# Kernel optimization log

Measured on AMD Instinct MI355X. Metric: run time of the kernel, lower is better.

Reference implementation:

```python
import jax, jax.numpy as jnp
import numpy as np

N_NODES = 100000
N_EDGES = 1600000
N_GRAPHS = 1000
H = 4

def _ln(x, g, b, eps=1e-5):
    m = x.mean(-1, keepdims=True)
    v = ((x - m) ** 2).mean(-1, keepdims=True)
    return (x - m) / jnp.sqrt(v + eps) * g + b

def _gat(x, src, dst, W, att_src, att_dst, bias, C):
    # PyG GATConv (self-loops already appended to src/dst): per-edge scores,
    # segment softmax over incoming edges of each dst node, scatter-add aggregation.
    N = x.shape[0]
    h = (x @ W.T).reshape(N, H, C)                      # [N,H,C]
    a_s = (h * att_src[None]).sum(-1)                   # [N,H]
    a_d = (h * att_dst[None]).sum(-1)                   # [N,H]
    e = jax.nn.leaky_relu(a_s[src] + a_d[dst], 0.2)     # [E,H]
    m = jax.ops.segment_max(e, dst, num_segments=N)
    w = jnp.exp(e - m[dst])
    denom = jax.ops.segment_sum(w, dst, num_segments=N)
    alpha = w / denom[dst]
    out = jax.ops.segment_sum(alpha[:, :, None] * h[src], dst, num_segments=N)
    return out.reshape(N, H * C) + bias

def _mha_len1(y, in_w, in_b, out_w, out_b, d):
    # seq_len==1 (x.unsqueeze(0)): softmax over a single key is identically 1,
    # so MHA(y,y,y) == out_proj(v_proj(y)). Exactly the original math.
    v = y @ in_w[2 * d:3 * d].T + in_b[2 * d:3 * d]
    return v @ out_w.T + out_b

def _forward(x, edge_index, batch, fc_feat_w, fc_feat_b,
             gat1_w, gat1_as, gat1_ad, gat1_b,
             gat2_w, gat2_as, gat2_ad, gat2_b,
             enc_in_w, enc_in_b, enc_out_w, enc_out_b,
             enc_f1_w, enc_f1_b, enc_f2_w, enc_f2_b,
             enc_ln1_g, enc_ln1_b, enc_ln2_g, enc_ln2_b,
             dec_sa_in_w, dec_sa_in_b, dec_sa_out_w, dec_sa_out_b,
             dec_ca_in_w, dec_ca_in_b, dec_ca_out_w, dec_ca_out_b,
             dec_f1_w, dec_f1_b, dec_f2_w, dec_f2_b,
             dec_ln1_g, dec_ln1_b, dec_ln2_g, dec_ln2_b, dec_ln3_g, dec_ln3_b,
             fc_w, fc_b):
    N = x.shape[0]
    d = 16 * H  # 64
    loop = jnp.arange(N, dtype=edge_index.dtype)
    src = jnp.concatenate([edge_index[0], loop])  # add_self_loops=True (PyG default)
    dst = jnp.concatenate([edge_index[1], loop])
    h = x @ fc_feat_w.T + fc_feat_b                     # feature_fc: [N,8]
    h = jax.nn.leaky_relu(_gat(h, src, dst, gat1_w, gat1_as, gat1_ad, gat1_b, 32), 0.01)
    h = jax.nn.leaky_relu(_gat(h, src, dst, gat2_w, gat2_as, gat2_ad, gat2_b, 16), 0.01)
    y = h  # [N,64]; transformer sees (L=1, B=N, E=64)
    for i in range(2):  # encoder layers
        a = _mha_len1(y, enc_in_w[i], enc_in_b[i], enc_out_w[i], enc_out_b[i], d)
        y = _ln(y + a, enc_ln1_g[i], enc_ln1_b[i])
        f = jax.nn.relu(y @ enc_f1_w[i].T + enc_f1_b[i]) @ enc_f2_w[i].T + enc_f2_b[i]
        y = _ln(y + f, enc_ln2_g[i], enc_ln2_b[i])
    for i in range(2):  # decoder layers (memory == tgt)
        a = _mha_len1(y, dec_sa_in_w[i], dec_sa_in_b[i], dec_sa_out_w[i], dec_sa_out_b[i], d)
        y = _ln(y + a, dec_ln1_g[i], dec_ln1_b[i])
        a = _mha_len1(y, dec_ca_in_w[i], dec_ca_in_b[i], dec_ca_out_w[i], dec_ca_out_b[i], d)
        y = _ln(y + a, dec_ln2_g[i], dec_ln2_b[i])
        f = jax.nn.relu(y @ dec_f1_w[i].T + dec_f1_b[i]) @ dec_f2_w[i].T + dec_f2_b[i]
        y = _ln(y + f, dec_ln3_g[i], dec_ln3_b[i])
    sums = jax.ops.segment_sum(y, batch, num_segments=N_GRAPHS)
    cnts = jax.ops.segment_sum(jnp.ones((N,), y.dtype), batch, num_segments=N_GRAPHS)
    pooled = sums / jnp.maximum(cnts, 1.0)[:, None]     # global_mean_pool
    return pooled @ fc_w.T + fc_b

def setup_inputs() -> dict:
    key = jax.random.key(0)
    ks = iter(jax.random.split(key, 64))
    p = lambda *s: jax.random.normal(next(ks), s, dtype=jnp.float32) * 0.1
    d = 64
    inp = {
        'x': jax.random.normal(next(ks), (N_NODES, 4), dtype=jnp.float32),
        'edge_index': jax.random.randint(next(ks), (2, N_EDGES), 0, N_NODES, dtype=jnp.int32),
        'batch': jnp.sort(jax.random.randint(next(ks), (N_NODES,), 0, N_GRAPHS, dtype=jnp.int32)),
        'fc_feat_w': p(8, 4), 'fc_feat_b': p(8),
        'gat1_w': p(128, 8), 'gat1_as': p(H, 32), 'gat1_ad': p(H, 32), 'gat1_b': p(128),
        'gat2_w': p(64, 128), 'gat2_as': p(H, 16), 'gat2_ad': p(H, 16), 'gat2_b': p(64),
        'enc_in_w': p(2, 3 * d, d), 'enc_in_b': p(2, 3 * d), 'enc_out_w': p(2, d, d), 'enc_out_b': p(2, d),
        'enc_f1_w': p(2, 256, d), 'enc_f1_b': p(2, 256), 'enc_f2_w': p(2, d, 256), 'enc_f2_b': p(2, d),
        'enc_ln1_g': jnp.ones((2, d)), 'enc_ln1_b': jnp.zeros((2, d)),
        'enc_ln2_g': jnp.ones((2, d)), 'enc_ln2_b': jnp.zeros((2, d)),
        'dec_sa_in_w': p(2, 3 * d, d), 'dec_sa_in_b': p(2, 3 * d), 'dec_sa_out_w': p(2, d, d), 'dec_sa_out_b': p(2, d),
        'dec_ca_in_w': p(2, 3 * d, d), 'dec_ca_in_b': p(2, 3 * d), 'dec_ca_out_w': p(2, d, d), 'dec_ca_out_b': p(2, d),
        'dec_f1_w': p(2, 256, d), 'dec_f1_b': p(2, 256), 'dec_f2_w': p(2, d, 256), 'dec_f2_b': p(2, d),
        'dec_ln1_g': jnp.ones((2, d)), 'dec_ln1_b': jnp.zeros((2, d)),
        'dec_ln2_g': jnp.ones((2, d)), 'dec_ln2_b': jnp.zeros((2, d)),
        'dec_ln3_g': jnp.ones((2, d)), 'dec_ln3_b': jnp.zeros((2, d)),
        'fc_w': p(33, d), 'fc_b': p(33),
    }
    return inp

def reference(x, edge_index, batch, fc_feat_w, fc_feat_b,
              gat1_w, gat1_as, gat1_ad, gat1_b,
              gat2_w, gat2_as, gat2_ad, gat2_b,
              enc_in_w, enc_in_b, enc_out_w, enc_out_b,
              enc_f1_w, enc_f1_b, enc_f2_w, enc_f2_b,
              enc_ln1_g, enc_ln1_b, enc_ln2_g, enc_ln2_b,
              dec_sa_in_w, dec_sa_in_b, dec_sa_out_w, dec_sa_out_b,
              dec_ca_in_w, dec_ca_in_b, dec_ca_out_w, dec_ca_out_b,
              dec_f1_w, dec_f1_b, dec_f2_w, dec_f2_b,
              dec_ln1_g, dec_ln1_b, dec_ln2_g, dec_ln2_b, dec_ln3_g, dec_ln3_b,
              fc_w, fc_b):
    return _forward(x, edge_index, batch, fc_feat_w, fc_feat_b,
                    gat1_w, gat1_as, gat1_ad, gat1_b,
                    gat2_w, gat2_as, gat2_ad, gat2_b,
                    enc_in_w, enc_in_b, enc_out_w, enc_out_b,
                    enc_f1_w, enc_f1_b, enc_f2_w, enc_f2_b,
                    enc_ln1_g, enc_ln1_b, enc_ln2_g, enc_ln2_b,
                    dec_sa_in_w, dec_sa_in_b, dec_sa_out_w, dec_sa_out_b,
                    dec_ca_in_w, dec_ca_in_b, dec_ca_out_w, dec_ca_out_b,
                    dec_f1_w, dec_f1_b, dec_f2_w, dec_f2_b,
                    dec_ln1_g, dec_ln1_b, dec_ln2_g, dec_ln2_b, dec_ln3_g, dec_ln3_b,
                    fc_w, fc_b)
```

## Files before the change

### kernel.cpp

```cpp
#include <hip/hip_runtime.h>

#define NN 100000
#define NE 1600000
#define NG 1000
#define ETOT (NE + NN)
#define NODES_PER_GRP 12500

typedef _Float16 f16x8 __attribute__((ext_vector_type(8)));
typedef _Float16 f16x4 __attribute__((ext_vector_type(4)));
typedef _Float16 f16x2 __attribute__((ext_vector_type(2)));
typedef float f32x16 __attribute__((ext_vector_type(16)));
#define XROW 72

__global__ void k_h1(const float* __restrict__ x, const float* __restrict__ ffw,
                     const float* __restrict__ ffb, const float* __restrict__ g1w,
                     const float* __restrict__ asw, const float* __restrict__ adw,
                     _Float16* __restrict__ h1p, float* __restrict__ asp,
                     float* __restrict__ ad_) {
    int tid = blockIdx.x * 256 + threadIdx.x;
    int n = __builtin_amdgcn_readfirstlane(tid >> 6);
    int jp = threadIdx.x & 63;
    float xv[4];
#pragma unroll
    for (int k = 0; k < 4; k++) xv[k] = x[n * 4 + k];
    float h0[8];
#pragma unroll
    for (int o = 0; o < 8; o++) {
        float a = ffb[o];
#pragma unroll
        for (int k = 0; k < 4; k++) a = fmaf(xv[k], ffw[o * 4 + k], a);
        h0[o] = a;
    }
    const float* w0 = g1w + jp * 8;
    const float* w1 = g1w + (jp + 64) * 8;
    float a0 = 0.f, a1 = 0.f;
#pragma unroll
    for (int k = 0; k < 8; k++) { a0 = fmaf(h0[k], w0[k], a0); a1 = fmaf(h0[k], w1[k], a1); }
    f16x2 r; r[0] = (_Float16)a0; r[1] = (_Float16)a1;
    *(f16x2*)(h1p + ((size_t)n * 64 + jp) * 2) = r;
    float p0 = a0 * asw[jp], p1 = a1 * asw[jp + 64];
    float d0 = a0 * adw[jp], d1 = a1 * adw[jp + 64];
#pragma unroll
    for (int m = 1; m <= 16; m <<= 1) {
        p0 += __shfl_xor(p0, m, 64); p1 += __shfl_xor(p1, m, 64);
        d0 += __shfl_xor(d0, m, 64); d1 += __shfl_xor(d1, m, 64);
    }
    if ((jp & 31) == 0) {
        int half = jp >> 5;
        *(float2*)(asp + n * 4 + half * 2) = make_float2(p0, p1);
        ad_[n * 4 + half] = d0;
        ad_[n * 4 + 2 + half] = d1;
    }
}

__global__ void k_att2(const _Float16* __restrict__ h2h, const float* __restrict__ asw,
                       const float* __restrict__ adw, float* __restrict__ as_,
                       float* __restrict__ ad_) {
    int tid = blockIdx.x * 256 + threadIdx.x;
    if (tid >= NN * 4) return;
    int n = tid >> 2, h = tid & 3;
    const _Float16* hp = h2h + (size_t)n * 64 + h * 16;
    const float* ws_ = asw + h * 16;
    const float* wd_ = adw + h * 16;
    float a = 0.f, d = 0.f;
#pragma unroll
    for (int c = 0; c < 16; c++) {
        float hv = (float)hp[c];
        a = fmaf(hv, ws_[c], a); d = fmaf(hv, wd_[c], d);
    }
    as_[tid] = a; ad_[tid] = d;
}

__global__ void k_count(const int* __restrict__ ei, int* __restrict__ deg) {
    int g = blockIdx.x & 7;
    int bi = blockIdx.x >> 3;
    int nb = gridDim.x >> 3;
    int lo = g * NODES_PER_GRP, hi = lo + NODES_PER_GRP;
    for (int e = bi * 256 + threadIdx.x; e < NE; e += nb * 256) {
        int dst = __builtin_nontemporal_load(ei + NE + e);
        if (dst >= lo && dst < hi) atomicAdd(&deg[dst], 1);
    }
}

__global__ void k_scan1(const int* __restrict__ deg, int* __restrict__ offs, int* __restrict__ bsum) {
    __shared__ int s[1024];
    int tid = threadIdx.x;
    int i = blockIdx.x * 1024 + tid;
    int v = (i < NN) ? deg[i] + 1 : 0;
    s[tid] = v;
    __syncthreads();
    for (int d = 1; d < 1024; d <<= 1) {
        int t = 0;
        if (tid >= d) t = s[tid - d];
        __syncthreads();
        if (tid >= d) s[tid] += t;
        __syncthreads();
    }
    if (i < NN) offs[i] = s[tid] - v;
    if (tid == 1023) bsum[blockIdx.x] = s[tid];
}

__global__ void k_scan2(int* __restrict__ bsum) {
    __shared__ int s[128];
    int tid = threadIdx.x;
    int v = (tid < 98) ? bsum[tid] : 0;
    s[tid] = v;
    __syncthreads();
    for (int d = 1; d < 128; d <<= 1) {
        int t = 0;
        if (tid >= d) t = s[tid - d];
        __syncthreads();
        if (tid >= d) s[tid] += t;
        __syncthreads();
    }
    bsum[tid] = s[tid] - v;
}

__global__ void k_scan3(int* __restrict__ offs, const int* __restrict__ bsum, int* __restrict__ cur,
                        int* __restrict__ srcs) {
    int i = blockIdx.x * 1024 + threadIdx.x;
    if (i < NN) {
        int v = offs[i] + bsum[blockIdx.x];
        offs[i] = v;
        cur[i] = v + 1;
        srcs[v] = i;
    }
    if (i == 0) offs[NN] = ETOT;
}

__global__ void k_scatter(const int* __restrict__ ei, int* __restrict__ cur,
                          int* __restrict__ srcs) {
    int g = blockIdx.x & 7;
    int bi = blockIdx.x >> 3;
    int nb = gridDim.x >> 3;
    int lo = g * NODES_PER_GRP, hi = lo + NODES_PER_GRP;
    for (int e = bi * 256 + threadIdx.x; e < NE; e += nb * 256) {
        int dst = __builtin_nontemporal_load(ei + NE + e);
        if (dst >= lo && dst < hi) {
            int src = __builtin_nontemporal_load(ei + e);
            int p = atomicAdd(&cur[dst], 1);
            srcs[p] = src;
        }
    }
}

__global__ void k_ew1(const int* __restrict__ offs, const int* __restrict__ srcs,
                      const float* __restrict__ asp, const float* __restrict__ ad_,
                      uint2* __restrict__ ew) {
    int t = blockIdx.x * 256 + threadIdx.x;
    int d = t >> 4, li = t & 15;
    if (d >= NN) return;
    int off = offs[d], deg = offs[d + 1] - off;
    float4 b = *(const float4*)(ad_ + d * 4);
    for (int j = li; j < deg; j += 16) {
        int s = srcs[off + j];
        float4 a = *(const float4*)(asp + s * 4);
        float e0 = a.x + b.x; e0 = fmaxf(e0, 0.2f * e0);
        float e2 = a.y + b.z; e2 = fmaxf(e2, 0.2f * e2);
        float e1 = a.z + b.y; e1 = fmaxf(e1, 0.2f * e1);
        float e3 = a.w + b.w; e3 = fmaxf(e3, 0.2f * e3);
        union { unsigned u; _Float16 h[2]; } c0, c1;
        c0.h[0] = (_Float16)__expf(e0); c0.h[1] = (_Float16)__expf(e2);
        c1.h[0] = (_Float16)__expf(e1); c1.h[1] = (_Float16)__expf(e3);
        uint2 o; o.x = c0.u; o.y = c1.u;
        ew[off + j] = o;
    }
}

__global__ void k_ew2(const int* __restrict__ offs, const int* __restrict__ srcs,
                      const float* __restrict__ as_, const float* __restrict__ ad_,
                      uint2* __restrict__ ew) {
    int t = blockIdx.x * 256 + threadIdx.x;
    int d = t >> 4, li = t & 15;
    if (d >= NN) return;
    int off = offs[d], deg = offs[d + 1] - off;
    float4 b = *(const float4*)(ad_ + d * 4);
    for (int j = li; j < deg; j += 16) {
        int s = srcs[off + j];
        float4 a = *(const float4*)(as_ + s * 4);
        float e0 = a.x + b.x; e0 = fmaxf(e0, 0.2f * e0);
        float e1 = a.y + b.y; e1 = fmaxf(e1, 0.2f * e1);
        float e2 = a.z + b.z; e2 = fmaxf(e2, 0.2f * e2);
        float e3 = a.w + b.w; e3 = fmaxf(e3, 0.2f * e3);
        union { unsigned u; _Float16 h[2]; } c0, c1;
        c0.h[0] = (_Float16)__expf(e0); c0.h[1] = (_Float16)__expf(e1);
        c1.h[0] = (_Float16)__expf(e2); c1.h[1] = (_Float16)__expf(e3);
        uint2 o; o.x = c0.u; o.y = c1.u;
        ew[off + j] = o;
    }
}

#define G1LD(q)  int s##q = sp[j + q]; uint2 e##q = wp[j + q];
#define G1LDM(q) int jj##q = j + q; int jc##q = jj##q < deg ? jj##q : deg - 1; \
                 int s##q = sp[jc##q]; uint2 e##q = wp[jc##q]; \
                 if (jj##q >= deg) { e##q.x = 0u; e##q.y = 0u; }
#define G1GA(q)  f16x2 p##q = *(const f16x2*)(h1p + (size_t)s##q * 128 + lane * 2);
#define G1AC(q, W0, W1, A0, A1) { \
    union { unsigned u; _Float16 h[2]; } c; c.u = hA ? e##q.y : e##q.x; \
    float w0 = (float)c.h[0], w1 = (float)c.h[1]; \
    W0 += w0; W1 += w1; \
    A0 = fmaf(w0, (float)p##q[0], A0); A1 = fmaf(w1, (float)p##q[1], A1); }

__global__ void k_gat1(const int* __restrict__ offs, const int* __restrict__ srcs,
                       const uint2* __restrict__ ew, const _Float16* __restrict__ h1p,
                       const float* __restrict__ bias, _Float16* __restrict__ g1h) {
    int wid = __builtin_amdgcn_readfirstlane((blockIdx.x * 256 + threadIdx.x) >> 6);
    int lane = threadIdx.x & 63;
    if (wid >= NN) return;
    int off = offs[wid];
    int deg = offs[wid + 1] - off;
    int hA = lane >> 5;
    const int* sp = srcs + off;
    const uint2* wp = ew + off;
    float ws0 = 0.f, ws1 = 0.f, ac0 = 0.f, ac1 = 0.f;
    float ws0b = 0.f, ws1b = 0.f, ac0b = 0.f, ac1b = 0.f;
    int j = 0;
    for (; j + 8 <= deg; j += 8) {
        G1LD(0) G1LD(1) G1LD(2) G1LD(3) G1LD(4) G1LD(5) G1LD(6) G1LD(7)
        G1GA(0) G1GA(1) G1GA(2) G1GA(3) G1GA(4) G1GA(5) G1GA(6) G1GA(7)
        G1AC(0, ws0, ws1, ac0, ac1)     G1AC(1, ws0b, ws1b, ac0b, ac1b)
        G1AC(2, ws0, ws1, ac0, ac1)     G1AC(3, ws0b, ws1b, ac0b, ac1b)
        G1AC(4, ws0, ws1, ac0, ac1)     G1AC(5, ws0b, ws1b, ac0b, ac1b)
        G1AC(6, ws0, ws1, ac0, ac1)     G1AC(7, ws0b, ws1b, ac0b, ac1b)
    }
    if (j < deg) {
        G1LDM(0) G1LDM(1) G1LDM(2) G1LDM(3) G1LDM(4) G1LDM(5) G1LDM(6) G1LDM(7)
        G1GA(0) G1GA(1) G1GA(2) G1GA(3) G1GA(4) G1GA(5) G1GA(6) G1GA(7)
        G1AC(0, ws0, ws1, ac0, ac1)     G1AC(1, ws0b, ws1b, ac0b, ac1b)
        G1AC(2, ws0, ws1, ac0, ac1)     G1AC(3, ws0b, ws1b, ac0b, ac1b)
        G1AC(4, ws0, ws1, ac0, ac1)     G1AC(5, ws0b, ws1b, ac0b, ac1b)
        G1AC(6, ws0, ws1, ac0, ac1)     G1AC(7, ws0b, ws1b, ac0b, ac1b)
    }
    ws0 += ws0b; ws1 += ws1b; ac0 += ac0b; ac1 += ac1b;
    float v0 = ac0 / ws0 + bias[lane];      v0 = fmaxf(v0, 0.01f * v0);
    float v1 = ac1 / ws1 + bias[lane + 64]; v1 = fmaxf(v1, 0.01f * v1);
    g1h[(size_t)wid * 128 + lane] = (_Float16)v0;
    g1h[(size_t)wid * 128 + lane + 64] = (_Float16)v1;
}

#define G2LD(q)  int s##q = sp[j + q]; uint2 e##q = wp[j + q];
#define G2LDM(q) int jj##q = j + q; int jc##q = jj##q < deg ? jj##q : deg - 1; \
                 int s##q = sp[jc##q]; uint2 e##q = wp[jc##q]; \
                 if (jj##q >= deg) { e##q.x = 0u; e##q.y = 0u; }
#define G2GA(q)  float hv##q = (float)h2h[(size_t)s##q * 64 + lane];
#define G2AC(q, W, A) { \
    unsigned sel = (hd & 2) ? e##q.y : e##q.x; \
    union { unsigned u; _Float16 h[2]; } c; c.u = sel >> sh; \
    float w = (float)c.h[0]; W += w; A = fmaf(w, hv##q, A); }

__global__ void k_gat2(const int* __restrict__ offs, const int* __restrict__ srcs,
                       const uint2* __restrict__ ew, const _Float16* __restrict__ h2h,
                       const float* __restrict__ bias, _Float16* __restrict__ g2h) {
    int wid = __builtin_amdgcn_readfirstlane((blockIdx.x * 256 + threadIdx.x) >> 6);
    int lane = threadIdx.x & 63;
    if (wid >= NN) return;
    int off = offs[wid];
    int deg = offs[wid + 1] - off;
    int hd = lane >> 4;
    int sh = (hd & 1) * 16;
    const int* sp = srcs + off;
    const uint2* wp = ew + off;
    float ws = 0.f, ac = 0.f, wsb = 0.f, acb = 0.f;
    int j = 0;
    for (; j + 8 <= deg; j += 8) {
        G2LD(0) G2LD(1) G2LD(2) G2LD(3) G2LD(4) G2LD(5) G2LD(6) G2LD(7)
        G2GA(0) G2GA(1) G2GA(2) G2GA(3) G2GA(4) G2GA(5) G2GA(6) G2GA(7)
        G2AC(0, ws, ac)  G2AC(1, wsb, acb)
        G2AC(2, ws, ac)  G2AC(3, wsb, acb)
        G2AC(4, ws, ac)  G2AC(5, wsb, acb)
        G2AC(6, ws, ac)  G2AC(7, wsb, acb)
    }
    if (j < deg) {
        G2LDM(0) G2LDM(1) G2LDM(2) G2LDM(3) G2LDM(4) G2LDM(5) G2LDM(6) G2LDM(7)
        G2GA(0) G2GA(1) G2GA(2) G2GA(3) G2GA(4) G2GA(5) G2GA(6) G2GA(7)
        G2AC(0, ws, ac)  G2AC(1, wsb, acb)
        G2AC(2, ws, ac)  G2AC(3, wsb, acb)
        G2AC(4, ws, ac)  G2AC(5, wsb, acb)
        G2AC(6, ws, ac)  G2AC(7, wsb, acb)
    }
    ws += wsb; ac += acb;
    float v = ac / ws + bias[lane]; v = fmaxf(v, 0.01f * v);
    g2h[(size_t)wid * 64 + lane] = (_Float16)v;
}

#define GROW 136
#define CROW 72
__global__ __launch_bounds__(256, 2) void k_h2m(const _Float16* __restrict__ g1h,
                                                const _Float16* __restrict__ apw2,
                                                _Float16* __restrict__ h2h) {
    __shared__ _Float16 ls[4 * 32 * GROW];
    const int t = threadIdx.x;
    const int w = t >> 6, l = t & 63;
    const int col = l & 31, hf = l >> 5;
    const int wv = blockIdx.x * 4 + w;
    const int nb = wv * 32;
    if (nb >= NN) return;
    _Float16* g16 = ls + w * (32 * GROW);
    const int r = l >> 1, hb = l & 1;
    {
        int nr = nb + r; if (nr >= NN) nr = NN - 1;
        const _Float16* src = g1h + (size_t)nr * 128 + hb * 64;
        _Float16* dst = g16 + r * GROW + hb * 64;
#pragma unroll
        for (int q = 0; q < 8; q++)
            *(f16x8*)(dst + q * 8) = *(const f16x8*)(src + q * 8);
    }
    f16x8 bf[8];
#pragma unroll
    for (int ks = 0; ks < 8; ks++)
        bf[ks] = *(const f16x8*)(g16 + col * GROW + ks * 16 + hf * 8);
    f32x16 acc0, acc1;
#pragma unroll
    for (int i = 0; i < 16; i++) { acc0[i] = 0.f; acc1[i] = 0.f; }
#pragma unroll
    for (int ks = 0; ks < 8; ks++) {
        f16x8 a0 = *(const f16x8*)(apw2 + ((0 * 8 + ks) * 64 + l) * 8);
        f16x8 a1 = *(const f16x8*)(apw2 + ((1 * 8 + ks) * 64 + l) * 8);
        acc0 = __builtin_amdgcn_mfma_f32_32x32x16_f16(a0, bf[ks], acc0, 0, 0, 0);
        acc1 = __builtin_amdgcn_mfma_f32_32x32x16_f16(a1, bf[ks], acc1, 0, 0, 0);
    }
    _Float16* c16 = g16;
#pragma unroll
    for (int rg = 0; rg < 4; rg++) {
        f16x4 h0, h1;
#pragma unroll
        for (int i = 0; i < 4; i++) { h0[i] = (_Float16)acc0[rg * 4 + i]; h1[i] = (_Float16)acc1[rg * 4 + i]; }
        *(f16x4*)(c16 + col * CROW + rg * 8 + hf * 4) = h0;
        *(f16x4*)(c16 + col * CROW + 32 + rg * 8 + hf * 4) = h1;
    }
    if (nb + r < NN) {
        _Float16* dst = h2h + (size_t)(nb + r) * 64 + hb * 32;
        const _Float16* srow = c16 + r * CROW + hb * 32;
#pragma unroll
        for (int q = 0; q < 4; q++)
            *(f16x8*)(dst + q * 8) = *(const f16x8*)(srow + q * 8);
    }
}

__global__ void k_fuse(const float* __restrict__ enc_in_w, const float* __restrict__ enc_in_b,
                       const float* __restrict__ enc_out_w, const float* __restrict__ enc_out_b,
                       const float* __restrict__ sa_in_w, const float* __restrict__ sa_in_b,
                       const float* __restrict__ sa_out_w, const float* __restrict__ sa_out_b,
                       const float* __restrict__ ca_in_w, const float* __restrict__ ca_in_b,
                       const float* __restrict__ ca_out_w, const float* __restrict__ ca_out_b,
                       _Float16* __restrict__ apk, float* __restrict__ fb) {
    int tid = blockIdx.x * 256 + threadIdx.x;
    int p = tid >> 12, r = tid & 4095, j = r >> 6, k = r & 63;
    int li = p & 1;
    const float *iw, *ib, *ow, *ob;
    if (p < 2)      { iw = enc_in_w + li * 12288; ib = enc_in_b + li * 192; ow = enc_out_w + li * 4096; ob = enc_out_b + li * 64; }
    else if (p < 4) { iw = sa_in_w + li * 12288;  ib = sa_in_b + li * 192;  ow = sa_out_w + li * 4096;  ob = sa_out_b + li * 64; }
    else            { iw = ca_in_w + li * 12288;  ib = ca_in_b + li * 192;  ow = ca_out_w + li * 4096;  ob = ca_out_b + li * 64; }
    float a = 0.f;
    for (int m = 0; m < 64; m++) a = fmaf(ow[j * 64 + m], iw[(128 + m) * 64 + k], a);
    int l = ((k >> 3) & 1) * 32 + (j & 31);
    apk[p * 4096 + (((j >> 5) * 4 + (k >> 4)) * 64 + l) * 8 + (k & 7)] = (_Float16)a;
    if (k == 0) {
        float fa = ob[j];
        for (int m = 0; m < 64; m++) fa = fmaf(ow[j * 64 + m], ib[128 + m], fa);
        fb[p * 64 + j] = fa;
    }
}

#define APK_F1 24576
#define APK_F2 90112
#define APK_TOT 155648
__global__ void k_apack(const float* __restrict__ ef1, const float* __restrict__ df1,
                        const float* __restrict__ ef2, const float* __restrict__ df2,
                        const float* __restrict__ g2w, _Float16* __restrict__ apk,
                        _Float16* __restrict__ apw2) {
    int tid = blockIdx.x * 256 + threadIdx.x;
    if (tid < 65536) {
        int pl = tid >> 14, idx = tid & 16383;
        int mt = idx >> 11, ks = (idx >> 9) & 3, l = (idx >> 3) & 63, d = idx & 7;
        int m = mt * 32 + (l & 31), k = ks * 16 + (l >> 5) * 8 + d;
        const float* f1 = (pl < 2) ? ef1 + pl * 16384 : df1 + (pl - 2) * 16384;
        apk[APK_F1 + pl * 16384 + idx] = (_Float16)f1[m * 64 + k];
    } else if (tid < 131072) {
        int r = tid - 65536;
        int pl = r >> 14, idx = r & 16383;
        int mt = idx >> 13, ks = (idx >> 9) & 15, l = (idx >> 3) & 63, d = idx & 7;
        int m = mt * 32 + (l & 31), k = ks * 16 + (l >> 5) * 8 + d;
        const float* f2 = (pl < 2) ? ef2 + pl * 16384 : df2 + (pl - 2) * 16384;
        apk[APK_F2 + pl * 16384 + idx] = (_Float16)f2[m * 256 + k];
    } else {
        int r = tid - 131072;
        int mtks = r >> 9, l = (r >> 3) & 63, d = r & 7;
        int mt = mtks >> 3, ks = mtks & 7;
        int m = mt * 32 + (l & 31), k = ks * 16 + (l >> 5) * 8 + d;
        apw2[r] = (_Float16)g2w[m * 128 + k];
    }
}

struct XQ {
    const _Float16* apk; const float* fb;
    const float* ef1b; const float* ef2b; const float* df1b; const float* df2b;
    const float* el1g; const float* el1b; const float* el2g; const float* el2b;
    const float* dl1g; const float* dl1b; const float* dl2g; const float* dl2b;
    const float* dl3g; const float* dl3b;
};

__device__ __forceinline__ void xstore(_Float16* xw, const float y[4][16], int col, int hf) {
#pragma unroll
    for (int nt = 0; nt < 2; nt++)
#pragma unroll
        for (int mt = 0; mt < 2; mt++)
#pragma unroll
            for (int rg = 0; rg < 4; rg++) {
                f16x4 h4;
#pragma unroll
                for (int i = 0; i < 4; i++) h4[i] = (_Float16)y[mt * 2 + nt][rg * 4 + i];
                *(f16x4*)(xw + (nt * 32 + col) * XROW + mt * 32 + rg * 8 + hf * 4) = h4;
            }
}

__device__ __forceinline__ void loadbf(const _Float16* xw, f16x8 bf[2][4], int col, int hf) {
#pragma unroll
    for (int nt = 0; nt < 2; nt++)
#pragma unroll
        for (int ks = 0; ks < 4; ks++)
            bf[nt][ks] = *(const f16x8*)(xw + (nt * 32 + col) * XROW + ks * 16 + hf * 8);
}

__device__ __forceinline__ void lnw(float y[4][16], const float* g, const float* b, int hf) {
#pragma unroll
    for (int nt = 0; nt < 2; nt++) {
        float s = 0.f, q = 0.f;
#pragma unroll
        for (int mt = 0; mt < 2; mt++)
#pragma unroll
            for (int r = 0; r < 16; r++) { float v = y[mt * 2 + nt][r]; s += v; q = fmaf(v, v, q); }
        s += __shfl_xor(s, 32, 64);
        q += __shfl_xor(q, 32, 64);
        float m = s * 0.015625f;
        float var = fmaf(q, 0.015625f, -m * m);
        float rs = rsqrtf(var + 1e-5f);
#pragma unroll
        for (int mt = 0; mt < 2; mt++)
#pragma unroll
            for (int rg = 0; rg < 4; rg++) {
                float4 g4 = *(const float4*)(g + mt * 32 + rg * 8 + hf * 4);
                float4 b4 = *(const float4*)(b + mt * 32 + rg * 8 + hf * 4);
                float* yp = &y[mt * 2 + nt][rg * 4];
                yp[0] = fmaf((yp[0] - m) * rs, g4.x, b4.x);
                yp[1] = fmaf((yp[1] - m) * rs, g4.y, b4.y);
                yp[2] = fmaf((yp[2] - m) * rs, g4.z, b4.z);
                yp[3] = fmaf((yp[3] - m) * rs, g4.w, b4.w);
            }
    }
}

__global__ __launch_bounds__(256, 2) void k_xform(const _Float16* __restrict__ yin,
                                                  float* __restrict__ yout, XQ P) {
    __shared__ _Float16 xs[4 * 64 * XROW];
    __shared__ _Float16 wb[8192];
    const int t = threadIdx.x;
    const int w = t >> 6, l = t & 63;
    const int col = l & 31, hf = l >> 5;
    _Float16* xw = xs + w * (64 * XROW);
    const int nb = blockIdx.x * 256 + w * 64;
    const int nn0 = nb + col, nn1 = nb + 32 + col;
    const int nc0 = nn0 < NN ? nn0 : NN - 1;
    const int nc1 = nn1 < NN ? nn1 : NN - 1;

    float y[4][16];
#pragma unroll
    for (int mt = 0; mt < 2; mt++)
#pragma unroll
        for (int nt = 0; nt < 2; nt++) {
            const _Float16* src = yin + (size_t)(nt ? nc1 : nc0) * 64 + mt * 32 + hf * 4;
#pragma unroll
            for (int rg = 0; rg < 4; rg++) {
                f16x4 v = *(const f16x4*)(src + rg * 8);
#pragma unroll
                for (int i = 0; i < 4; i++) y[mt * 2 + nt][rg * 4 + i] = (float)v[i];
            }
        }
    f16x8 bf[2][4];
    xstore(xw, y, col, hf);
    loadbf(xw, bf, col, hf);

#pragma unroll 1
    for (int layer = 0; layer < 4; layer++) {
        const bool enc = layer < 2;
        const int li = enc ? layer : layer - 2;
        const int nat = enc ? 1 : 2;
#pragma unroll 1
        for (int at = 0; at < nat; at++) {
            const int p = enc ? layer : (at == 0 ? 2 + li : 4 + li);
            const _Float16* apA = P.apk + p * 4096;
            __syncthreads();
#pragma unroll
            for (int i = 0; i < 2; i++)
                *(f16x8*)(wb + (t + i * 256) * 8) = *(const f16x8*)(apA + (t + i * 256) * 8);
            __syncthreads();
            const float* fbp = P.fb + p * 64;
            f32x16 acc[4];
#pragma unroll
            for (int mt = 0; mt < 2; mt++) {
                f32x16 a;
#pragma unroll
                for (int rg = 0; rg < 4; rg++) {
                    float4 b4 = *(const float4*)(fbp + mt * 32 + rg * 8 + hf * 4);
                    a[rg * 4 + 0] = b4.x; a[rg * 4 + 1] = b4.y; a[rg * 4 + 2] = b4.z; a[rg * 4 + 3] = b4.w;
                }
                acc[mt * 2 + 0] = a; acc[mt * 2 + 1] = a;
            }
#pragma unroll
            for (int mt = 0; mt < 2; mt++)
#pragma unroll
                for (int ks = 0; ks < 4; ks++) {
                    f16x8 af = *(const f16x8*)(wb + ((mt * 4 + ks) * 64 + l) * 8);
                    acc[mt * 2 + 0] = __builtin_amdgcn_mfma_f32_32x32x16_f16(af, bf[0][ks], acc[mt * 2 + 0], 0, 0, 0);
                    acc[mt * 2 + 1] = __builtin_amdgcn_mfma_f32_32x32x16_f16(af, bf[1][ks], acc[mt * 2 + 1], 0, 0, 0);
                }
#pragma unroll
            for (int ti = 0; ti < 4; ti++)
#pragma unroll
                for (int r = 0; r < 16; r++) y[ti][r] += acc[ti][r];
            const float *g, *b;
            if (enc)          { g = P.el1g + li * 64; b = P.el1b + li * 64; }
            else if (at == 0) { g = P.dl1g + li * 64; b = P.dl1b + li * 64; }
            else              { g = P.dl2g + li * 64; b = P.dl2b + li * 64; }
            lnw(y, g, b, hf);
            xstore(xw, y, col, hf);
            loadbf(xw, bf, col, hf);
        }
        const int pl = enc ? layer : 2 + li;
        const _Float16* apF1 = P.apk + APK_F1 + pl * 16384;
        const _Float16* apF2 = P.apk + APK_F2 + pl * 16384;
        const float* f1bp = (enc ? P.ef1b : P.df1b) + li * 256;
        const float* f2bp = (enc ? P.ef2b : P.df2b) + li * 64;
        f32x16 out[4];
#pragma unroll
        for (int mt = 0; mt < 2; mt++) {
            f32x16 a;
#pragma unroll
            for (int rg = 0; rg < 4; rg++) {
                float4 b4 = *(const float4*)(f2bp + mt * 32 + rg * 8 + hf * 4);
                a[rg * 4 + 0] = b4.x; a[rg * 4 + 1] = b4.y; a[rg * 4 + 2] = b4.z; a[rg * 4 + 3] = b4.w;
            }
            out[mt * 2 + 0] = a; out[mt * 2 + 1] = a;
        }
#pragma unroll 1
        for (int c = 0; c < 4; c++) {
            __syncthreads();
#pragma unroll
            for (int i = 0; i < 2; i++)
                *(f16x8*)(wb + (t + i * 256) * 8) = *(const f16x8*)(apF1 + c * 4096 + (t + i * 256) * 8);
            *(f16x8*)(wb + 4096 + t * 8) = *(const f16x8*)(apF2 + c * 2048 + t * 8);
            *(f16x8*)(wb + 6144 + t * 8) = *(const f16x8*)(apF2 + 8192 + c * 2048 + t * 8);
            __syncthreads();
            f32x16 ha[4];
#pragma unroll
            for (int hmt = 0; hmt < 2; hmt++) {
                f32x16 a;
#pragma unroll
                for (int rg = 0; rg < 4; rg++) {
                    float4 b4 = *(const float4*)(f1bp + c * 64 + hmt * 32 + rg * 8 + hf * 4);
                    a[rg * 4 + 0] = b4.x; a[rg * 4 + 1] = b4.y; a[rg * 4 + 2] = b4.z; a[rg * 4 + 3] = b4.w;
                }
                ha[hmt * 2 + 0] = a; ha[hmt * 2 + 1] = a;
            }
#pragma unroll
            for (int hmt = 0; hmt < 2; hmt++)
#pragma unroll
                for (int ks = 0; ks < 4; ks++) {
                    f16x8 af = *(const f16x8*)(wb + ((hmt * 4 + ks) * 64 + l) * 8);
                    ha[hmt * 2 + 0] = __builtin_amdgcn_mfma_f32_32x32x16_f16(af, bf[0][ks], ha[hmt * 2 + 0], 0, 0, 0);
                    ha[hmt * 2 + 1] = __builtin_amdgcn_mfma_f32_32x32x16_f16(af, bf[1][ks], ha[hmt * 2 + 1], 0, 0, 0);
                }
#pragma unroll
            for (int nt = 0; nt < 2; nt++)
#pragma unroll
                for (int hmt = 0; hmt < 2; hmt++)
#pragma unroll
                    for (int rg = 0; rg < 4; rg++) {
                        f16x4 h4;
#pragma unroll
                        for (int i = 0; i < 4; i++)
                            h4[i] = (_Float16)fmaxf(ha[hmt * 2 + nt][rg * 4 + i], 0.f);
                        *(f16x4*)(xw + (nt * 32 + col) * XROW + hmt * 32 + rg * 8 + hf * 4) = h4;
                    }
#pragma unroll
            for (int ksl = 0; ksl < 4; ksl++) {
                f16x8 hbf0 = *(const f16x8*)(xw + col * XROW + ksl * 16 + hf * 8);
                f16x8 hbf1 = *(const f16x8*)(xw + (32 + col) * XROW + ksl * 16 + hf * 8);
#pragma unroll
                for (int mt = 0; mt < 2; mt++) {
                    f16x8 af = *(const f16x8*)(wb + 4096 + mt * 2048 + (ksl * 64 + l) * 8);
                    out[mt * 2 + 0] = __builtin_amdgcn_mfma_f32_32x32x16_f16(af, hbf0, out[mt * 2 + 0], 0, 0, 0);
                    out[mt * 2 + 1] = __builtin_amdgcn_mfma_f32_32x32x16_f16(af, hbf1, out[mt * 2 + 1], 0, 0, 0);
                }
            }
        }
#pragma unroll
        for (int ti = 0; ti < 4; ti++)
#pragma unroll
            for (int r = 0; r < 16; r++) y[ti][r] += out[ti][r];
        const float* g2 = (enc ? P.el2g : P.dl3g) + li * 64;
        const float* b2 = (enc ? P.el2b : P.dl3b) + li * 64;
        lnw(y, g2, b2, hf);
        if (layer < 3) {
            xstore(xw, y, col, hf);
            loadbf(xw, bf, col, hf);
        }
    }
#pragma unroll
    for (int mt = 0; mt < 2; mt++)
#pragma unroll
        for (int nt = 0; nt < 2; nt++) {
            int n = nt ? nn1 : nn0;
            if (n < NN) {
                float* dst = yout + (size_t)n * 64 + mt * 32 + hf * 4;
#pragma unroll
                for (int rg = 0; rg < 4; rg++) {
                    const float* yp = &y[mt * 2 + nt][rg * 4];
                    *(float4*)(dst + rg * 8) = make_float4(yp[0], yp[1], yp[2], yp[3]);
                }
            }
        }
}

__global__ void k_pool(const float* __restrict__ y, const int* __restrict__ batch,
                       float* __restrict__ pooled) {
    int b = blockIdx.x;
    int t = threadIdx.x;
    int ch = t & 63, r = t >> 6;
    int lo = 0, hi = NN;
    while (lo < hi) { int mid = (lo + hi) >> 1; if (batch[mid] < b) lo = mid + 1; else hi = mid; }
    int st = lo;
    hi = NN;
    while (lo < hi) { int mid = (lo + hi) >> 1; if (batch[mid] < b + 1) lo = mid + 1; else hi = mid; }
    int en = lo;
    float s = 0.f;
    for (int i = st + r; i < en; i += 4) s += y[(size_t)i * 64 + ch];
    __shared__ float red[256];
    red[t] = s;
    __syncthreads();
    if (t < 64) {
        float tot = red[t] + red[t + 64] + red[t + 128] + red[t + 192];
        int cnt = en - st; if (cnt < 1) cnt = 1;
        pooled[b * 64 + t] = tot / (float)cnt;
    }
}

__global__ void k_fc(const float* __restrict__ pooled, const float* __restrict__ fcw,
                     const float* __restrict__ fcb, float* __restrict__ out) {
    int tid = blockIdx.x * 256 + threadIdx.x;
    if (tid >= NG * 33) return;
    int g = tid / 33, o = tid - g * 33;
    const float* p = pooled + g * 64;
    const float* w = fcw + o * 64;
    float a0 = 0.f, a1 = 0.f, a2 = 0.f, a3 = 0.f;
#pragma unroll
    for (int k = 0; k < 16; k++) {
        a0 = fmaf(p[4 * k], w[4 * k], a0);
        a1 = fmaf(p[4 * k + 1], w[4 * k + 1], a1);
        a2 = fmaf(p[4 * k + 2], w[4 * k + 2], a2);
        a3 = fmaf(p[4 * k + 3], w[4 * k + 3], a3);
    }
    out[tid] = fcb[o] + (a0 + a1) + (a2 + a3);
}

extern "C" void kernel_launch(void* const* d_in, const int* in_sizes, int n_in,
                              void* d_out, int out_size, void* d_ws, size_t ws_size,
                              hipStream_t stream) {
    (void)in_sizes; (void)n_in; (void)out_size; (void)ws_size;
    char* ws = (char*)d_ws;
    size_t o = 0;
    auto A = [&](size_t b) { size_t r = o; o += (b + 255) & ~(size_t)255; return r; };
    _Float16* h1p = (_Float16*)(ws + A((size_t)NN * 128 * 2));
    _Float16* h2h = (_Float16*)(ws + A((size_t)NN * 64 * 2));
    _Float16* g1h = (_Float16*)(ws + A((size_t)NN * 128 * 2));
    _Float16* g2h = (_Float16*)(ws + A((size_t)NN * 64 * 2));
    float* f_y   = (float*)(ws + A((size_t)NN * 64 * 4));
    float* f_asp = (float*)(ws + A((size_t)NN * 4 * 4));
    float* f_ad1 = (float*)(ws + A((size_t)NN * 4 * 4));
    float* f_as2 = (float*)(ws + A((size_t)NN * 4 * 4));
    float* f_ad2 = (float*)(ws + A((size_t)NN * 4 * 4));
    int* i_off   = (int*)(ws + A((size_t)(NN + 1) * 4));
    int* i_cur   = (int*)(ws + A((size_t)NN * 4));
    int* i_deg   = (int*)(ws + A((size_t)NN * 4));
    int* i_bsum  = (int*)(ws + A((size_t)1024 * 4));
    int* i_srcs  = (int*)(ws + A((size_t)ETOT * 4));
    uint2* e_w   = (uint2*)(ws + A((size_t)ETOT * 8));
    float* f_fb  = (float*)(ws + A((size_t)6 * 64 * 4));
    _Float16* f_apk = (_Float16*)(ws + A((size_t)APK_TOT * 2));
    _Float16* apw2  = (_Float16*)(ws + A((size_t)8192 * 2));
    float* f_pool= (float*)(ws + A((size_t)NG * 64 * 4));

    const float* x   = (const float*)d_in[0];
    const int* ei    = (const int*)d_in[1];
    const int* batch = (const int*)d_in[2];
    #define F32(i) ((const float*)d_in[i])

    hipMemsetAsync(i_deg, 0, (size_t)NN * 4, stream);
    k_h1<<<NN * 64 / 256, 256, 0, stream>>>(x, F32(3), F32(4), F32(5), F32(6), F32(7),
                                            h1p, f_asp, f_ad1);
    k_count<<<8 * 128, 256, 0, stream>>>(ei, i_deg);
    k_scan1<<<98, 1024, 0, stream>>>(i_deg, i_off, i_bsum);
    k_scan2<<<1, 128, 0, stream>>>(i_bsum);
    k_scan3<<<98, 1024, 0, stream>>>(i_off, i_bsum, i_cur, i_srcs);
    k_scatter<<<8 * 128, 256, 0, stream>>>(ei, i_cur, i_srcs);
    k_ew1<<<NN * 16 / 256, 256, 0, stream>>>(i_off, i_srcs, f_asp, f_ad1, e_w);
    k_gat1<<<NN * 64 / 256, 256, 0, stream>>>(i_off, i_srcs, e_w, h1p, F32(8), g1h);
    k_apack<<<544, 256, 0, stream>>>(F32(17), F32(33), F32(19), F32(35), F32(9), f_apk, apw2);
    k_h2m<<<(NN / 32 + 3) / 4, 256, 0, stream>>>(g1h, apw2, h2h);
    k_att2<<<(NN * 4 + 255) / 256, 256, 0, stream>>>(h2h, F32(10), F32(11), f_as2, f_ad2);
    k_ew2<<<NN * 16 / 256, 256, 0, stream>>>(i_off, i_srcs, f_as2, f_ad2, e_w);
    k_gat2<<<NN * 64 / 256, 256, 0, stream>>>(i_off, i_srcs, e_w, h2h, F32(12), g2h);
    k_fuse<<<24576 / 256, 256, 0, stream>>>(F32(13), F32(14), F32(15), F32(16),
                                            F32(25), F32(26), F32(27), F32(28),
                                            F32(29), F32(30), F32(31), F32(32),
                                            f_apk, f_fb);
    XQ Q;
    Q.apk = f_apk; Q.fb = f_fb;
    Q.ef1b = F32(18); Q.ef2b = F32(20);
    Q.df1b = F32(34); Q.df2b = F32(36);
    Q.el1g = F32(21); Q.el1b = F32(22); Q.el2g = F32(23); Q.el2b = F32(24);
    Q.dl1g = F32(37); Q.dl1b = F32(38); Q.dl2g = F32(39); Q.dl2b = F32(40);
    Q.dl3g = F32(41); Q.dl3b = F32(42);
    k_xform<<<(NN + 255) / 256, 256, 0, stream>>>(g2h, f_y, Q);
    k_pool<<<NG, 256, 0, stream>>>(f_y, batch, f_pool);
    k_fc<<<(NG * 33 + 255) / 256, 256, 0, stream>>>(f_pool, F32(43), F32(44), (float*)d_out);
    #undef F32
}
```

Before: 585.9 us.

## Unroll edge count/scatter loops and shrink xform blocks to two waves

The degree-count and CSR-scatter kernels now unroll their grid-stride loops by four, issuing several independent edge loads before the atomics, and launch twice as many blocks. The transformer kernel drops from four waves to two per block, with half the LDS for activations and weight-staging loops adjusted for 128 threads, and twice as many blocks. The intent is more memory-level parallelism in the graph-building atomics and more resident blocks for k_xform on the CUs. The cost is that each k_xform block repeats the weight staging for fewer nodes, and the scatter kernel holds more live registers.

```diff
diff --git a/kernel.cpp b/kernel.cpp
--- a/kernel.cpp
+++ b/kernel.cpp
@@ -76,9 +76,17 @@
     int bi = blockIdx.x >> 3;
     int nb = gridDim.x >> 3;
     int lo = g * NODES_PER_GRP, hi = lo + NODES_PER_GRP;
-    for (int e = bi * 256 + threadIdx.x; e < NE; e += nb * 256) {
-        int dst = __builtin_nontemporal_load(ei + NE + e);
-        if (dst >= lo && dst < hi) atomicAdd(&deg[dst], 1);
+    int stride = nb * 256;
+    for (int e = bi * 256 + threadIdx.x; e < NE; e += 4 * stride) {
+        int e1 = e + stride, e2 = e + 2 * stride, e3 = e + 3 * stride;
+        int d0 = __builtin_nontemporal_load(ei + NE + e);
+        int d1 = (e1 < NE) ? __builtin_nontemporal_load(ei + NE + e1) : -1;
+        int d2 = (e2 < NE) ? __builtin_nontemporal_load(ei + NE + e2) : -1;
+        int d3 = (e3 < NE) ? __builtin_nontemporal_load(ei + NE + e3) : -1;
+        if (d0 >= lo && d0 < hi) atomicAdd(&deg[d0], 1);
+        if (d1 >= lo && d1 < hi) atomicAdd(&deg[d1], 1);
+        if (d2 >= lo && d2 < hi) atomicAdd(&deg[d2], 1);
+        if (d3 >= lo && d3 < hi) atomicAdd(&deg[d3], 1);
     }
 }
 
@@ -134,13 +142,19 @@
     int bi = blockIdx.x >> 3;
     int nb = gridDim.x >> 3;
     int lo = g * NODES_PER_GRP, hi = lo + NODES_PER_GRP;
-    for (int e = bi * 256 + threadIdx.x; e < NE; e += nb * 256) {
-        int dst = __builtin_nontemporal_load(ei + NE + e);
-        if (dst >= lo && dst < hi) {
-            int src = __builtin_nontemporal_load(ei + e);
-            int p = atomicAdd(&cur[dst], 1);
-            srcs[p] = src;
-        }
+    int stride = nb * 256;
+    for (int e = bi * 256 + threadIdx.x; e < NE; e += 4 * stride) {
+        int e1 = e + stride, e2 = e + 2 * stride, e3 = e + 3 * stride;
+        int d0 = __builtin_nontemporal_load(ei + NE + e);
+        int s0 = __builtin_nontemporal_load(ei + e);
+        int d1 = -1, s1 = 0, d2 = -1, s2 = 0, d3 = -1, s3 = 0;
+        if (e1 < NE) { d1 = __builtin_nontemporal_load(ei + NE + e1); s1 = __builtin_nontemporal_load(ei + e1); }
+        if (e2 < NE) { d2 = __builtin_nontemporal_load(ei + NE + e2); s2 = __builtin_nontemporal_load(ei + e2); }
+        if (e3 < NE) { d3 = __builtin_nontemporal_load(ei + NE + e3); s3 = __builtin_nontemporal_load(ei + e3); }
+        if (d0 >= lo && d0 < hi) { int p = atomicAdd(&cur[d0], 1); srcs[p] = s0; }
+        if (d1 >= lo && d1 < hi) { int p = atomicAdd(&cur[d1], 1); srcs[p] = s1; }
+        if (d2 >= lo && d2 < hi) { int p = atomicAdd(&cur[d2], 1); srcs[p] = s2; }
+        if (d3 >= lo && d3 < hi) { int p = atomicAdd(&cur[d3], 1); srcs[p] = s3; }
     }
 }
 
@@ -450,15 +464,15 @@
     }
 }
 
-__global__ __launch_bounds__(256, 2) void k_xform(const _Float16* __restrict__ yin,
+__global__ __launch_bounds__(128, 2) void k_xform(const _Float16* __restrict__ yin,
                                                   float* __restrict__ yout, XQ P) {
-    __shared__ _Float16 xs[4 * 64 * XROW];
+    __shared__ _Float16 xs[2 * 64 * XROW];
     __shared__ _Float16 wb[8192];
     const int t = threadIdx.x;
     const int w = t >> 6, l = t & 63;
     const int col = l & 31, hf = l >> 5;
     _Float16* xw = xs + w * (64 * XROW);
-    const int nb = blockIdx.x * 256 + w * 64;
+    const int nb = blockIdx.x * 128 + w * 64;
     const int nn0 = nb + col, nn1 = nb + 32 + col;
     const int nc0 = nn0 < NN ? nn0 : NN - 1;
     const int nc1 = nn1 < NN ? nn1 : NN - 1;
@@ -491,8 +505,8 @@
             const _Float16* apA = P.apk + p * 4096;
             __syncthreads();
 #pragma unroll
-            for (int i = 0; i < 2; i++)
-                *(f16x8*)(wb + (t + i * 256) * 8) = *(const f16x8*)(apA + (t + i * 256) * 8);
+            for (int i = 0; i < 4; i++)
+                *(f16x8*)(wb + (t + i * 128) * 8) = *(const f16x8*)(apA + (t + i * 128) * 8);
             __syncthreads();
             const float* fbp = P.fb + p * 64;
             f32x16 acc[4];
@@ -546,10 +560,13 @@
         for (int c = 0; c < 4; c++) {
             __syncthreads();
 #pragma unroll
-            for (int i = 0; i < 2; i++)
-                *(f16x8*)(wb + (t + i * 256) * 8) = *(const f16x8*)(apF1 + c * 4096 + (t + i * 256) * 8);
-            *(f16x8*)(wb + 4096 + t * 8) = *(const f16x8*)(apF2 + c * 2048 + t * 8);
-            *(f16x8*)(wb + 6144 + t * 8) = *(const f16x8*)(apF2 + 8192 + c * 2048 + t * 8);
+            for (int i = 0; i < 4; i++)
+                *(f16x8*)(wb + (t + i * 128) * 8) = *(const f16x8*)(apF1 + c * 4096 + (t + i * 128) * 8);
+#pragma unroll
+            for (int i = 0; i < 2; i++) {
+                *(f16x8*)(wb + 4096 + (t + i * 128) * 8) = *(const f16x8*)(apF2 + c * 2048 + (t + i * 128) * 8);
+                *(f16x8*)(wb + 6144 + (t + i * 128) * 8) = *(const f16x8*)(apF2 + 8192 + c * 2048 + (t + i * 128) * 8);
+            }
             __syncthreads();
             f32x16 ha[4];
 #pragma unroll
@@ -698,11 +715,11 @@
     hipMemsetAsync(i_deg, 0, (size_t)NN * 4, stream);
     k_h1<<<NN * 64 / 256, 256, 0, stream>>>(x, F32(3), F32(4), F32(5), F32(6), F32(7),
                                             h1p, f_asp, f_ad1);
-    k_count<<<8 * 128, 256, 0, stream>>>(ei, i_deg);
+    k_count<<<8 * 256, 256, 0, stream>>>(ei, i_deg);
     k_scan1<<<98, 1024, 0, stream>>>(i_deg, i_off, i_bsum);
     k_scan2<<<1, 128, 0, stream>>>(i_bsum);
     k_scan3<<<98, 1024, 0, stream>>>(i_off, i_bsum, i_cur, i_srcs);
-    k_scatter<<<8 * 128, 256, 0, stream>>>(ei, i_cur, i_srcs);
+    k_scatter<<<8 * 256, 256, 0, stream>>>(ei, i_cur, i_srcs);
     k_ew1<<<NN * 16 / 256, 256, 0, stream>>>(i_off, i_srcs, f_asp, f_ad1, e_w);
     k_gat1<<<NN * 64 / 256, 256, 0, stream>>>(i_off, i_srcs, e_w, h1p, F32(8), g1h);
     k_apack<<<544, 256, 0, stream>>>(F32(17), F32(33), F32(19), F32(35), F32(9), f_apk, apw2);
@@ -721,7 +738,7 @@
     Q.el1g = F32(21); Q.el1b = F32(22); Q.el2g = F32(23); Q.el2b = F32(24);
     Q.dl1g = F32(37); Q.dl1b = F32(38); Q.dl2g = F32(39); Q.dl2b = F32(40);
     Q.dl3g = F32(41); Q.dl3b = F32(42);
-    k_xform<<<(NN + 255) / 256, 256, 0, stream>>>(g2h, f_y, Q);
+    k_xform<<<(NN + 127) / 128, 128, 0, stream>>>(g2h, f_y, Q);
     k_pool<<<NG, 256, 0, stream>>>(f_y, batch, f_pool);
     k_fc<<<(NG * 33 + 255) / 256, 256, 0, stream>>>(f_pool, F32(43), F32(44), (float*)d_out);
     #undef F32
```

Result: no change. 591.4 us (+0.9%).
